# Kernel tuning notes

Measured on AMD Instinct MI355X. Metric: run time of the kernel, lower is better.

Reference implementation:

```python
import jax, jax.numpy as jnp
import numpy as np
import math

B, S, D, H = 4, 2048, 1024, 16
DK = D // H


def _rope_tables(seq_len, dim, dtype=jnp.float32):
    inv_freq = 1.0 / (10000.0 ** (jnp.arange(0, dim, 2, dtype=jnp.float32) / dim))
    t = jnp.arange(seq_len, dtype=jnp.float32)
    freqs = jnp.einsum('i,j->ij', t, inv_freq)          # [S, dim/2]
    emb = jnp.concatenate([freqs, freqs], axis=-1)       # [S, dim]
    return jnp.cos(emb).astype(dtype)[None, None], jnp.sin(emb).astype(dtype)[None, None]


def _apply_rope(x, cos, sin):
    # faithful to source: rotated = cat([-x[...,1::2], x[...,::2]], -1)
    x_rot = jnp.concatenate([-x[..., 1::2], x[..., ::2]], axis=-1)
    return x * cos + x_rot * sin


def setup_inputs() -> dict:
    key = jax.random.key(0)
    ks = jax.random.split(key, 12)
    scale = 1.0 / math.sqrt(D)
    inp = {
        'query': jax.random.normal(ks[0], (B, S, D), jnp.float32),
        'key':   jax.random.normal(ks[1], (B, S, D), jnp.float32),
        'value': jax.random.normal(ks[2], (B, S, D), jnp.float32),
        'mask':  jnp.tril(jnp.ones((S, S), jnp.int32))[None, None],  # causal [1,1,S,S]
        'w_q': jax.random.normal(ks[3], (D, D), jnp.float32) * scale,
        'b_q': jnp.zeros((D,), jnp.float32),
        'w_k': jax.random.normal(ks[4], (D, D), jnp.float32) * scale,
        'b_k': jnp.zeros((D,), jnp.float32),
        'w_v': jax.random.normal(ks[5], (D, D), jnp.float32) * scale,
        'b_v': jnp.zeros((D,), jnp.float32),
        'w_o': jax.random.normal(ks[6], (D, D), jnp.float32) * scale,
        'b_o': jnp.zeros((D,), jnp.float32),
    }
    return inp


def reference(query, key, value, mask, w_q, b_q, w_k, b_k, w_v, b_v, w_o, b_o):
    b, s, _ = query.shape
    # projections (torch Linear: x @ W.T + b), split heads -> [B,H,S,Dk]
    def proj(x, w, bias):
        return (x @ w.T + bias).reshape(b, -1, H, DK).transpose(0, 2, 1, 3)
    Q = proj(query, w_q, b_q)
    K = proj(key, w_k, b_k)
    V = proj(value, w_v, b_v)
    cos, sin = _rope_tables(s, DK, Q.dtype)
    Q = _apply_rope(Q, cos, sin)
    K = _apply_rope(K, cos, sin)
    scores = jnp.einsum('bhqd,bhkd->bhqk', Q, K) / math.sqrt(DK)
    scores = jnp.where(mask == 0, jnp.asarray(-1e9, scores.dtype), scores)
    attn = jax.nn.softmax(scores, axis=-1)
    ctx = jnp.einsum('bhqk,bhkd->bhqd', attn, V)
    ctx = ctx.transpose(0, 2, 1, 3).reshape(b, -1, D)
    return ctx @ w_o.T + b_o
```

## Files before the change

### kernel.cpp

```cpp
#include <hip/hip_runtime.h>
#include <hip/hip_bf16.h>
#include <math.h>

#define B_  4
#define S_  2048
#define D_  1024
#define H_  16
#define DK_ 64
#define M_  (B_ * S_)

typedef short short8 __attribute__((ext_vector_type(8)));
typedef float floatx4 __attribute__((ext_vector_type(4)));

__device__ inline unsigned short f2bf(float x) {
    unsigned u = __float_as_uint(x);
    u = (u + 0x7fff + ((u >> 16) & 1)) >> 16;
    return (unsigned short)u;
}
__device__ inline float bf2f(unsigned short h) {
    return __uint_as_float(((unsigned)h) << 16);
}

__device__ inline unsigned cvt_pk_bf16(float lo, float hi) {
    unsigned r;
    asm("v_cvt_pk_bf16_f32 %0, %1, %2" : "=v"(r) : "v"(lo), "v"(hi));
    return r;
}

template <int K>
__device__ inline float dpp_ror(float x) {
    return __uint_as_float((unsigned)__builtin_amdgcn_update_dpp(
        0, (int)__float_as_uint(x), 0x120 | K, 0xF, 0xF, true));
}
__device__ inline float rowmax16(float x) {
    x = fmaxf(x, dpp_ror<8>(x));
    x = fmaxf(x, dpp_ror<4>(x));
    x = fmaxf(x, dpp_ror<2>(x));
    x = fmaxf(x, dpp_ror<1>(x));
    return x;
}
__device__ inline float rowsum16(float x) {
    x += dpp_ror<8>(x);
    x += dpp_ror<4>(x);
    x += dpp_ror<2>(x);
    x += dpp_ror<1>(x);
    return x;
}

#define GLOAD_LDS16(g, l)                                          \
    __builtin_amdgcn_global_load_lds(                              \
        (const __attribute__((address_space(1))) void*)(g),        \
        (__attribute__((address_space(3))) void*)(l), 16, 0, 0)

__global__ __launch_bounds__(256) void cvt_inputs_kernel(
    const float* __restrict__ q, const float* __restrict__ k,
    const float* __restrict__ v, unsigned short* __restrict__ Ah)
{
    const int z = blockIdx.z;
    const float* src = (z == 0) ? q : (z == 1) ? k : v;
    unsigned short* dst = Ah + (size_t)z * M_ * D_;
    const size_t i = ((size_t)blockIdx.x * 256 + threadIdx.x) * 4;
    float4 f = *(const float4*)(src + i);
    ushort4 o;
    o.x = f2bf(f.x); o.y = f2bf(f.y); o.z = f2bf(f.z); o.w = f2bf(f.w);
    *(ushort4*)(dst + i) = o;
}

__global__ __launch_bounds__(256) void cvt_weights_kernel(
    const float* __restrict__ wq, const float* __restrict__ wk,
    const float* __restrict__ wv, const float* __restrict__ wo,
    unsigned short* __restrict__ Wh, unsigned short* __restrict__ Woh)
{
    const int z = blockIdx.z;
    const float* src = (z == 0) ? wq : (z == 1) ? wk : (z == 2) ? wv : wo;
    unsigned short* dst = (z < 3) ? (Wh + (size_t)z * D_ * D_) : Woh;
    const size_t i = ((size_t)blockIdx.x * 256 + threadIdx.x) * 4;
    float4 f = *(const float4*)(src + i);
    ushort4 o;
    o.x = f2bf(f.x); o.y = f2bf(f.y); o.z = f2bf(f.z); o.w = f2bf(f.w);
    *(ushort4*)(dst + i) = o;
}

template <int MODE>
__global__ __launch_bounds__(256) void gemm_bf16_kernel(
    const unsigned short* __restrict__ Ah, const unsigned short* __restrict__ Wh,
    const float* __restrict__ bq, const float* __restrict__ bk,
    const float* __restrict__ bv, void* __restrict__ outv)
{
    __shared__ __align__(16) unsigned short As[2][128 * 32];
    __shared__ __align__(16) unsigned short Bs[2][128 * 32];

    const int tid  = threadIdx.x;
    const int wave = tid >> 6;
    const int lane = tid & 63;
    const int quad = lane >> 4;
    const int l15  = lane & 15;
    const int z    = (MODE == 1) ? blockIdx.z : 0;
    const int m0   = blockIdx.x * 128;
    const int n0   = blockIdx.y * 128;
    const int wrow = (wave >> 1) * 64;
    const int wcol = (wave & 1) * 64;

    const unsigned short* A = Ah + (size_t)z * M_ * D_;
    const unsigned short* W = Wh + (size_t)z * D_ * D_;

    const int srow   = tid >> 2;
    const int schunk = (tid & 3) * 8;

#define STAGE_G(BUF, K0)                                                     \
    {                                                                        \
        GLOAD_LDS16(A + (size_t)(m0 + srow) * D_ + (K0) + schunk,            \
                    &As[BUF][wave * 512]);                                   \
        GLOAD_LDS16(W + (size_t)(n0 + srow) * D_ + (K0) + schunk,            \
                    &Bs[BUF][wave * 512]);                                   \
        GLOAD_LDS16(A + (size_t)(m0 + 64 + srow) * D_ + (K0) + schunk,       \
                    &As[BUF][2048 + wave * 512]);                            \
        GLOAD_LDS16(W + (size_t)(n0 + 64 + srow) * D_ + (K0) + schunk,       \
                    &Bs[BUF][2048 + wave * 512]);                            \
    }

    floatx4 acc[4][4] = {};

    STAGE_G(0, 0);
    __syncthreads();

    for (int k0 = 0; k0 < D_; k0 += 32) {
        const int cur = (k0 >> 5) & 1;
        if (k0 + 32 < D_) STAGE_G(cur ^ 1, k0 + 32);

        short8 af[4], bf[4];
#pragma unroll
        for (int i = 0; i < 4; ++i)
            af[i] = *(const short8*)&As[cur][(wrow + i * 16 + l15) * 32 + quad * 8];
#pragma unroll
        for (int j = 0; j < 4; ++j)
            bf[j] = *(const short8*)&Bs[cur][(wcol + j * 16 + l15) * 32 + quad * 8];
#pragma unroll
        for (int i = 0; i < 4; ++i)
#pragma unroll
            for (int j = 0; j < 4; ++j)
                acc[i][j] = __builtin_amdgcn_mfma_f32_16x16x32_bf16(
                    af[i], bf[j], acc[i][j], 0, 0, 0);

        __syncthreads();
    }
#undef STAGE_G

    const float* bias = (MODE == 0) ? bq : (z == 0) ? bq : (z == 1) ? bk : bv;

    if (MODE == 1) {
        unsigned short* Tw = (unsigned short*)As + wave * 16 * 68;
        const int bg = m0 >> 11;

        if (z == 2) {
            const int s0g = (m0 & (S_ - 1)) + wrow + quad * 16;
#pragma unroll
            for (int j = 0; j < 4; ++j) {
                const int n = n0 + wcol + j * 16 + l15;
                const float bn = bias[n];
#pragma unroll
                for (int i = 0; i < 4; ++i)
#pragma unroll
                    for (int reg = 0; reg < 4; ++reg)
                        Tw[l15 * 68 + i * 16 + quad * 4 + reg] =
                            f2bf(acc[i][j][reg] + bn);
                short8 r0 = *(const short8*)&Tw[l15 * 68 + quad * 16];
                short8 r1 = *(const short8*)&Tw[l15 * 68 + quad * 16 + 8];
                const int h = n >> 6, d = n & 63;
                unsigned short* dp = (unsigned short*)outv + 2 * (size_t)M_ * D_ +
                    (((size_t)(bg * H_ + h)) * DK_ + d) * S_ + s0g;
                *(short8*)(dp) = r0;
                *(short8*)(dp + 8) = r1;
            }
        } else {
            const int hq = (n0 + wcol) >> 6;
            const int sb = (m0 & (S_ - 1)) + wrow;
            unsigned short* dstz = (unsigned short*)outv + (size_t)z * M_ * D_;
#pragma unroll
            for (int i = 0; i < 4; ++i) {
#pragma unroll
                for (int j = 0; j < 4; ++j) {
                    const float bn = bias[n0 + wcol + j * 16 + l15];
#pragma unroll
                    for (int reg = 0; reg < 4; ++reg)
                        Tw[(quad * 4 + reg) * 68 + j * 16 + l15] =
                            f2bf(acc[i][j][reg] + bn);
                }
                short8 r0 = *(const short8*)&Tw[l15 * 68 + quad * 16];
                short8 r1 = *(const short8*)&Tw[l15 * 68 + quad * 16 + 8];
                unsigned short* dp = dstz +
                    (((size_t)bg * H_ + hq) * S_ + sb + i * 16 + l15) * DK_ +
                    quad * 16;
                *(short8*)dp = r0;
                *(short8*)(dp + 8) = r1;
            }
        }
        return;
    }

#pragma unroll
    for (int j = 0; j < 4; ++j) {
        const int n = n0 + wcol + j * 16 + l15;
        const float bn = bias[n];
#pragma unroll
        for (int i = 0; i < 4; ++i) {
#pragma unroll
            for (int reg = 0; reg < 4; ++reg) {
                const int m = m0 + wrow + i * 16 + quad * 4 + reg;
                ((float*)outv)[(size_t)m * D_ + n] = acc[i][j][reg] + bn;
            }
        }
    }
}

__global__ __launch_bounds__(256) void rope_tab_kernel(float* __restrict__ tab)
{
    const int idx = blockIdx.x * 256 + threadIdx.x;
    const int s = idx >> 5, j = idx & 31;
    const float inv_freq = exp2f((float)(2 * j) * (-13.28771237954945f / 64.f));
    const float ang = (float)s * inv_freq;
    tab[idx * 2]     = cosf(ang);
    tab[idx * 2 + 1] = sinf(ang);
}

__global__ __launch_bounds__(256) void rope_kernel(unsigned short* __restrict__ Q,
                                                   unsigned short* __restrict__ K,
                                                   const float* __restrict__ tab)
{
    const int wave = blockIdx.x * 4 + (threadIdx.x >> 6);
    const int lane = threadIdx.x & 63;
    const int rowsPer = B_ * H_ * S_;

    unsigned short* base = (wave < rowsPer) ? Q : K;
    const int row = (wave < rowsPer) ? wave : wave - rowsPer;
    const int s = row & (S_ - 1);

    unsigned short* p = base + (size_t)row * DK_;
    const float v = bf2f(p[lane]);

    const int j = lane & 31;
    const float2 cs = ((const float2*)tab)[s * 32 + j];

    const int partner = (lane < 32) ? (2 * lane + 1) : (2 * (lane - 32));
    const float sign = (lane < 32) ? -1.0f : 1.0f;
    const float pv = __shfl(v, partner);

    p[lane] = f2bf(v * cs.x + sign * pv * cs.y);
}

__global__ __launch_bounds__(256, 4) void attn_kernel(
    const unsigned short* __restrict__ Qh, const unsigned short* __restrict__ Kh,
    const unsigned short* __restrict__ Vt, unsigned short* __restrict__ ctx)
{
    __shared__ __align__(16) unsigned short Ks[2][64 * 64];
    __shared__ __align__(16) unsigned short Vs[2][64 * 64];
    __shared__ __align__(16) short Pw[4][16 * 64];

    const int tid  = threadIdx.x;
    const int wave = tid >> 6;
    const int lane = tid & 63;
    const int quad = lane >> 4;
    const int l15  = lane & 15;

    const int L  = blockIdx.x;
    const int bh = ((L >> 3) & 7) * 8 + (L & 7);
    const int qt = 31 - (L >> 6);
    const int q0 = qt * 64;

    const float c2 = 0.18033688011f;

    const unsigned short* Kbase = Kh + (size_t)bh * S_ * DK_;
    const unsigned short* Vbase = Vt + (size_t)bh * DK_ * S_;
    const int b = bh >> 4, h = bh & 15;

    short* Pme = &Pw[wave][0];

    const unsigned short* Qrow =
        Qh + ((size_t)bh * S_ + q0 + wave * 16 + l15) * DK_;
    short8 aQ[2];
    aQ[0] = *(const short8*)(Qrow + quad * 8);
    aQ[1] = *(const short8*)(Qrow + 32 + quad * 8);

    const int srow = lane >> 3;
    const int sg   = (lane & 7) ^ srow;
    const unsigned short* kSrc = Kbase + (size_t)(wave * 8 + srow) * DK_ + sg * 8;
    const unsigned short* vSrc = Vbase + (size_t)(wave * 8 + srow) * S_ + sg * 8;

    floatx4 acc[4] = {};
    float m_i[4] = {-INFINITY, -INFINITY, -INFINITY, -INFINITY};
    float l_i[4] = {0.f, 0.f, 0.f, 0.f};

#pragma unroll
    for (int rd = 0; rd < 2; ++rd) {
        GLOAD_LDS16(kSrc + (size_t)rd * 32 * DK_, &Ks[0][rd * 2048 + wave * 512]);
        GLOAD_LDS16(vSrc + (size_t)rd * 32 * S_,  &Vs[0][rd * 2048 + wave * 512]);
    }
    __syncthreads();

    int buf = 0;
    for (int j0 = 0; j0 <= q0; j0 += 64) {
        if (j0 + 64 <= q0) {
#pragma unroll
            for (int rd = 0; rd < 2; ++rd) {
                GLOAD_LDS16(kSrc + (size_t)(j0 + 64 + rd * 32) * DK_,
                            &Ks[buf ^ 1][rd * 2048 + wave * 512]);
                GLOAD_LDS16(vSrc + (j0 + 64) + (size_t)rd * 32 * S_,
                            &Vs[buf ^ 1][rd * 2048 + wave * 512]);
            }
        }

        floatx4 st[4] = {};
#pragma unroll
        for (int t = 0; t < 4; ++t)
#pragma unroll
            for (int kh = 0; kh < 2; ++kh) {
                short8 kf = *(const short8*)&Ks[buf][(t * 16 + l15) * 64 +
                              ((((kh << 2) + quad) ^ (l15 & 7)) << 3)];
                st[t] = __builtin_amdgcn_mfma_f32_16x16x32_bf16(
                    aQ[kh], kf, st[t], 0, 0, 0);
            }

        if (j0 == q0) {
#pragma unroll
            for (int t = 0; t < 4; ++t)
#pragma unroll
                for (int reg = 0; reg < 4; ++reg)
                    if (t * 16 + l15 > wave * 16 + quad * 4 + reg)
                        st[t][reg] = -INFINITY;
        }

#pragma unroll
        for (int reg = 0; reg < 4; ++reg) {
            float rmx = fmaxf(fmaxf(st[0][reg], st[1][reg]),
                              fmaxf(st[2][reg], st[3][reg]));
            rmx = rowmax16(rmx);
            const float pm = rmx * c2;
            if (__ballot(pm > m_i[reg] + 8.0f) != 0ull) {
                const float m2 = fmaxf(m_i[reg], pm);
                const float alpha = exp2f(m_i[reg] - m2);
                l_i[reg] *= alpha;
                m_i[reg] = m2;
                if (__ballot(alpha == 1.0f) != ~0ull) {
#pragma unroll
                    for (int t = 0; t < 4; ++t) acc[t][reg] *= alpha;
                }
            }
            const float m2v = m_i[reg];

            const float p0 = exp2f(fmaf(st[0][reg], c2, -m2v));
            const float p1 = exp2f(fmaf(st[1][reg], c2, -m2v));
            const float p2 = exp2f(fmaf(st[2][reg], c2, -m2v));
            const float p3 = exp2f(fmaf(st[3][reg], c2, -m2v));

            const unsigned pk01 = cvt_pk_bf16(p0, p1);
            const unsigned pk23 = cvt_pk_bf16(p2, p3);
            const int r   = quad * 4 + reg;
            const int sw  = r & 7;
            const int ghi = l15 >> 3;
            short* prow = Pme + r * 64 + (l15 & 7);
            prow[((0 + ghi) ^ sw) << 3] = (short)(unsigned short)pk01;
            prow[((2 + ghi) ^ sw) << 3] = (short)(unsigned short)(pk01 >> 16);
            prow[((4 + ghi) ^ sw) << 3] = (short)(unsigned short)pk23;
            prow[((6 + ghi) ^ sw) << 3] = (short)(unsigned short)(pk23 >> 16);

            float rs = (p0 + p1) + (p2 + p3);
            rs = rowsum16(rs);
            l_i[reg] += rs;
        }

#pragma unroll
        for (int kh = 0; kh < 2; ++kh) {
            short8 aP = *(const short8*)&Pme[l15 * 64 +
                          ((((kh << 2) + quad) ^ (l15 & 7)) << 3)];
#pragma unroll
            for (int t = 0; t < 4; ++t) {
                short8 vf = *(const short8*)&Vs[buf][(t * 16 + l15) * 64 +
                              ((((kh << 2) + quad) ^ (l15 & 7)) << 3)];
                acc[t] = __builtin_amdgcn_mfma_f32_16x16x32_bf16(
                    aP, vf, acc[t], 0, 0, 0);
            }
        }

        __syncthreads();
        buf ^= 1;
    }

#pragma unroll
    for (int reg = 0; reg < 4; ++reg) {
        const float inv = 1.0f / l_i[reg];
        const int q = q0 + wave * 16 + quad * 4 + reg;
        unsigned short* orow = ctx + ((size_t)b * S_ + q) * D_ + h * DK_;
#pragma unroll
        for (int t = 0; t < 4; ++t)
            orow[t * 16 + l15] = f2bf(acc[t][reg] * inv);
    }
}

extern "C" void kernel_launch(void* const* d_in, const int* in_sizes, int n_in,
                              void* d_out, int out_size, void* d_ws, size_t ws_size,
                              hipStream_t stream)
{
    const float* query = (const float*)d_in[0];
    const float* key   = (const float*)d_in[1];
    const float* value = (const float*)d_in[2];
    const float* w_q = (const float*)d_in[4];
    const float* b_q = (const float*)d_in[5];
    const float* w_k = (const float*)d_in[6];
    const float* b_k = (const float*)d_in[7];
    const float* w_v = (const float*)d_in[8];
    const float* b_v = (const float*)d_in[9];
    const float* w_o = (const float*)d_in[10];
    const float* b_o = (const float*)d_in[11];
    float* out = (float*)d_out;

    char* ws = (char*)d_ws;
    const size_t half = (size_t)M_ * D_ * sizeof(unsigned short);
    unsigned short* Ah   = (unsigned short*)(ws);
    unsigned short* Wh   = (unsigned short*)(ws + 3 * half);
    unsigned short* Woh  = (unsigned short*)(ws + 3 * half + 3 * half / 8);
    unsigned short* QKVb = (unsigned short*)(ws + 3 * half + 4 * half / 8);
    unsigned short* Ctxh = (unsigned short*)(ws + 6 * half + 4 * half / 8);
    float*          Rtab = (float*)ws;

    cvt_inputs_kernel<<<dim3(M_ * D_ / 1024, 1, 3), 256, 0, stream>>>(
        query, key, value, Ah);
    cvt_weights_kernel<<<dim3(D_ * D_ / 1024, 1, 4), 256, 0, stream>>>(
        w_q, w_k, w_v, w_o, Wh, Woh);

    gemm_bf16_kernel<1><<<dim3(M_ / 128, D_ / 128, 3), 256, 0, stream>>>(
        Ah, Wh, b_q, b_k, b_v, QKVb);

    unsigned short* Qb = QKVb;
    unsigned short* Kb = QKVb + (size_t)M_ * D_;
    unsigned short* Vb = QKVb + 2 * (size_t)M_ * D_;

    rope_tab_kernel<<<(S_ * 32) / 256, 256, 0, stream>>>(Rtab);
    rope_kernel<<<(2 * B_ * H_ * S_) / 4, 256, 0, stream>>>(Qb, Kb, Rtab);

    attn_kernel<<<dim3(2048), 256, 0, stream>>>(Qb, Kb, Vb, Ctxh);

    gemm_bf16_kernel<0><<<dim3(M_ / 128, D_ / 128, 1), 256, 0, stream>>>(
        Ctxh, Woh, b_o, b_o, b_o, out);
}
```

Before: 393.8 us.

## Fuse RoPE into QKV GEMM epilogue and fold table build into weight conversion

```diff
diff --git a/kernel.cpp b/kernel.cpp
--- a/kernel.cpp
+++ b/kernel.cpp
@@ -69,9 +69,21 @@
 __global__ __launch_bounds__(256) void cvt_weights_kernel(
     const float* __restrict__ wq, const float* __restrict__ wk,
     const float* __restrict__ wv, const float* __restrict__ wo,
-    unsigned short* __restrict__ Wh, unsigned short* __restrict__ Woh)
+    unsigned short* __restrict__ Wh, unsigned short* __restrict__ Woh,
+    float* __restrict__ tab)
 {
     const int z = blockIdx.z;
+    if (z == 4) {
+        if (blockIdx.x >= 256) return;
+        const int idx = blockIdx.x * 256 + threadIdx.x;
+        const int s = idx >> 5, j = idx & 31;
+        const float inv_freq =
+            exp2f((float)(2 * j) * (-13.28771237954945f / 64.f));
+        const float ang = (float)s * inv_freq;
+        tab[idx * 2]     = cosf(ang);
+        tab[idx * 2 + 1] = sinf(ang);
+        return;
+    }
     const float* src = (z == 0) ? wq : (z == 1) ? wk : (z == 2) ? wv : wo;
     unsigned short* dst = (z < 3) ? (Wh + (size_t)z * D_ * D_) : Woh;
     const size_t i = ((size_t)blockIdx.x * 256 + threadIdx.x) * 4;
@@ -85,7 +97,8 @@
 __global__ __launch_bounds__(256) void gemm_bf16_kernel(
     const unsigned short* __restrict__ Ah, const unsigned short* __restrict__ Wh,
     const float* __restrict__ bq, const float* __restrict__ bk,
-    const float* __restrict__ bv, void* __restrict__ outv)
+    const float* __restrict__ bv, void* __restrict__ outv,
+    const float* __restrict__ tab)
 {
     __shared__ __align__(16) unsigned short As[2][128 * 32];
     __shared__ __align__(16) unsigned short Bs[2][128 * 32];
@@ -176,6 +189,7 @@
             const int hq = (n0 + wcol) >> 6;
             const int sb = (m0 & (S_ - 1)) + wrow;
             unsigned short* dstz = (unsigned short*)outv + (size_t)z * M_ * D_;
+            const float sgn = (quad < 2) ? -1.f : 1.f;
 #pragma unroll
             for (int i = 0; i < 4; ++i) {
 #pragma unroll
@@ -186,13 +200,49 @@
                         Tw[(quad * 4 + reg) * 68 + j * 16 + l15] =
                             f2bf(acc[i][j][reg] + bn);
                 }
-                short8 r0 = *(const short8*)&Tw[l15 * 68 + quad * 16];
-                short8 r1 = *(const short8*)&Tw[l15 * 68 + quad * 16 + 8];
+                const unsigned short* Trow = Tw + l15 * 68;
+                uint4 xa = *(const uint4*)(Trow + quad * 16);
+                uint4 xb = *(const uint4*)(Trow + quad * 16 + 8);
+                const unsigned short* Prow = Trow + (quad & 1) * 32;
+                uint4 pa = *(const uint4*)(Prow);
+                uint4 pb = *(const uint4*)(Prow + 8);
+                uint4 pc = *(const uint4*)(Prow + 16);
+                uint4 pd = *(const uint4*)(Prow + 24);
+                const int s = sb + i * 16 + l15;
+                const float4* tb =
+                    (const float4*)tab + (s * 16 + (quad & 1) * 8);
+                const unsigned xw[8] = {xa.x, xa.y, xa.z, xa.w,
+                                        xb.x, xb.y, xb.z, xb.w};
+                const unsigned pw[16] = {pa.x, pa.y, pa.z, pa.w,
+                                         pb.x, pb.y, pb.z, pb.w,
+                                         pc.x, pc.y, pc.z, pc.w,
+                                         pd.x, pd.y, pd.z, pd.w};
+                unsigned ow[8];
+#pragma unroll
+                for (int c2 = 0; c2 < 8; ++c2) {
+                    const float4 cs = tb[c2];
+                    const float xe = __uint_as_float(xw[c2] << 16);
+                    const float xo = __uint_as_float(xw[c2] & 0xffff0000u);
+                    const unsigned pe = pw[2 * c2], po = pw[2 * c2 + 1];
+                    const float pre = (quad < 2)
+                        ? __uint_as_float(pe & 0xffff0000u)
+                        : __uint_as_float(pe << 16);
+                    const float pro = (quad < 2)
+                        ? __uint_as_float(po & 0xffff0000u)
+                        : __uint_as_float(po << 16);
+                    const float o0 = fmaf(pre, sgn * cs.y, xe * cs.x);
+                    const float o1 = fmaf(pro, sgn * cs.w, xo * cs.z);
+                    ow[c2] = cvt_pk_bf16(o0, o1);
+                }
                 unsigned short* dp = dstz +
                     (((size_t)bg * H_ + hq) * S_ + sb + i * 16 + l15) * DK_ +
                     quad * 16;
-                *(short8*)dp = r0;
-                *(short8*)(dp + 8) = r1;
+                uint4 olo; olo.x = ow[0]; olo.y = ow[1];
+                           olo.z = ow[2]; olo.w = ow[3];
+                uint4 ohi; ohi.x = ow[4]; ohi.y = ow[5];
+                           ohi.z = ow[6]; ohi.w = ow[7];
+                *(uint4*)dp = olo;
+                *(uint4*)(dp + 8) = ohi;
             }
         }
         return;
@@ -211,41 +261,6 @@
             }
         }
     }
-}
-
-__global__ __launch_bounds__(256) void rope_tab_kernel(float* __restrict__ tab)
-{
-    const int idx = blockIdx.x * 256 + threadIdx.x;
-    const int s = idx >> 5, j = idx & 31;
-    const float inv_freq = exp2f((float)(2 * j) * (-13.28771237954945f / 64.f));
-    const float ang = (float)s * inv_freq;
-    tab[idx * 2]     = cosf(ang);
-    tab[idx * 2 + 1] = sinf(ang);
-}
-
-__global__ __launch_bounds__(256) void rope_kernel(unsigned short* __restrict__ Q,
-                                                   unsigned short* __restrict__ K,
-                                                   const float* __restrict__ tab)
-{
-    const int wave = blockIdx.x * 4 + (threadIdx.x >> 6);
-    const int lane = threadIdx.x & 63;
-    const int rowsPer = B_ * H_ * S_;
-
-    unsigned short* base = (wave < rowsPer) ? Q : K;
-    const int row = (wave < rowsPer) ? wave : wave - rowsPer;
-    const int s = row & (S_ - 1);
-
-    unsigned short* p = base + (size_t)row * DK_;
-    const float v = bf2f(p[lane]);
-
-    const int j = lane & 31;
-    const float2 cs = ((const float2*)tab)[s * 32 + j];
-
-    const int partner = (lane < 32) ? (2 * lane + 1) : (2 * (lane - 32));
-    const float sign = (lane < 32) ? -1.0f : 1.0f;
-    const float pv = __shfl(v, partner);
-
-    p[lane] = f2bf(v * cs.x + sign * pv * cs.y);
 }
 
 __global__ __launch_bounds__(256, 4) void attn_kernel(
@@ -310,6 +325,7 @@
         }
 
         floatx4 st[4] = {};
+        __builtin_amdgcn_s_setprio(1);
 #pragma unroll
         for (int t = 0; t < 4; ++t)
 #pragma unroll
@@ -319,6 +335,7 @@
                 st[t] = __builtin_amdgcn_mfma_f32_16x16x32_bf16(
                     aQ[kh], kf, st[t], 0, 0, 0);
             }
+        __builtin_amdgcn_s_setprio(0);
 
         if (j0 == q0) {
 #pragma unroll
@@ -368,6 +385,7 @@
             l_i[reg] += rs;
         }
 
+        __builtin_amdgcn_s_setprio(1);
 #pragma unroll
         for (int kh = 0; kh < 2; ++kh) {
             short8 aP = *(const short8*)&Pme[l15 * 64 +
@@ -380,6 +398,7 @@
                     aP, vf, acc[t], 0, 0, 0);
             }
         }
+        __builtin_amdgcn_s_setprio(0);
 
         __syncthreads();
         buf ^= 1;
@@ -420,25 +439,22 @@
     unsigned short* Woh  = (unsigned short*)(ws + 3 * half + 3 * half / 8);
     unsigned short* QKVb = (unsigned short*)(ws + 3 * half + 4 * half / 8);
     unsigned short* Ctxh = (unsigned short*)(ws + 6 * half + 4 * half / 8);
-    float*          Rtab = (float*)ws;
+    float*          Rtab = (float*)Ctxh;
 
     cvt_inputs_kernel<<<dim3(M_ * D_ / 1024, 1, 3), 256, 0, stream>>>(
         query, key, value, Ah);
-    cvt_weights_kernel<<<dim3(D_ * D_ / 1024, 1, 4), 256, 0, stream>>>(
-        w_q, w_k, w_v, w_o, Wh, Woh);
+    cvt_weights_kernel<<<dim3(D_ * D_ / 1024, 1, 5), 256, 0, stream>>>(
+        w_q, w_k, w_v, w_o, Wh, Woh, Rtab);
 
     gemm_bf16_kernel<1><<<dim3(M_ / 128, D_ / 128, 3), 256, 0, stream>>>(
-        Ah, Wh, b_q, b_k, b_v, QKVb);
+        Ah, Wh, b_q, b_k, b_v, QKVb, Rtab);
 
     unsigned short* Qb = QKVb;
     unsigned short* Kb = QKVb + (size_t)M_ * D_;
     unsigned short* Vb = QKVb + 2 * (size_t)M_ * D_;
 
-    rope_tab_kernel<<<(S_ * 32) / 256, 256, 0, stream>>>(Rtab);
-    rope_kernel<<<(2 * B_ * H_ * S_) / 4, 256, 0, stream>>>(Qb, Kb, Rtab);
-
     attn_kernel<<<dim3(2048), 256, 0, stream>>>(Qb, Kb, Vb, Ctxh);
 
     gemm_bf16_kernel<0><<<dim3(M_ / 128, D_ / 128, 1), 256, 0, stream>>>(
-        Ctxh, Woh, b_o, b_o, b_o, out);
-}
+        Ctxh, Woh, b_o, b_o, b_o, out, Rtab);
+}
```

After: 373.1 us. 5.3% less time.
